# Optimization experiments

Hardware: AMD Instinct MI355X
Metric: run time of the kernel (lower is better)

## Reference

```python
import jax, jax.numpy as jnp
import numpy as np

B, S, D, H = 8, 1024, 1024, 16
DH = D // H  # 64

def setup_inputs() -> dict:
    key = jax.random.key(0)
    k1, k2, k3 = jax.random.split(key, 3)
    x = jax.random.normal(k1, (B, S, D), dtype=jnp.float32)
    mask = jnp.tril(jnp.ones((S, S), dtype=bool))[None, None]  # causal [1,1,S,S]
    W_qkv = jax.random.normal(k2, (D, 3 * D), dtype=jnp.float32) * 0.02
    W_out = jax.random.normal(k3, (D, D), dtype=jnp.float32) * 0.02
    return {"x": x, "mask": mask, "W_qkv": W_qkv, "W_out": W_out}

def reference(x, mask, W_qkv, W_out):
    qkv = jnp.einsum('bnd,de->bne', x, W_qkv)
    q, k, v = jnp.split(qkv, 3, axis=-1)
    # [b, h, n, dh]
    split_heads = lambda t: t.reshape(B, S, H, DH).transpose(0, 2, 1, 3)
    q, k, v = map(split_heads, (q, k, v))
    attn = jnp.einsum('bhnd,bhmd->bhnm', q, k) / jnp.sqrt(jnp.float32(DH))
    attn = jnp.where(mask, attn, 0.7 * jnp.finfo(attn.dtype).min)
    attn = jax.nn.softmax(attn.astype(jnp.float32), axis=-1).astype(x.dtype)
    out = jnp.einsum('bhnm,bhmd->bhnd', attn, v)
    out = out.transpose(0, 2, 1, 3).reshape(B, S, D)
    return jnp.einsum('bnd,de->bne', out, W_out)
```

## Files before the change

### kernel.cpp

```cpp
#include <hip/hip_runtime.h>
#include <stdint.h>

typedef __attribute__((ext_vector_type(8))) short short8;
typedef __attribute__((ext_vector_type(4))) float floatx4;

__device__ __forceinline__ unsigned short f2bf(float f) {
  union { float f; uint32_t u; } v; v.f = f;
  uint32_t u = v.u;
  return (unsigned short)((u + 0x7FFFu + ((u >> 16) & 1u)) >> 16);
}

__device__ __forceinline__ uint32_t fbits(float f) {
  union { float f; uint32_t u; } v; v.f = f; return v.u;
}
__device__ __forceinline__ uint32_t pkbf(float hi, float lo) {
  return __builtin_amdgcn_perm(fbits(hi), fbits(lo), 0x07060302u);
}

__device__ __forceinline__ void gl_lds16(const void* g, void* l) {
  __builtin_amdgcn_global_load_lds((__attribute__((address_space(1))) void*)g,
                                   (__attribute__((address_space(3))) void*)l,
                                   16, 0, 0);
}

__global__ __launch_bounds__(256) void prep_kernel(const float* __restrict__ x,
                                                   unsigned short* __restrict__ xb,
                                                   const float* __restrict__ Wqkv,
                                                   unsigned short* __restrict__ WqkvT,
                                                   const float* __restrict__ Wout,
                                                   unsigned short* __restrict__ WoutT) {
  __shared__ float tile[32][33];
  int id = blockIdx.x;
  if (id < 8192) {
    int i = id * 256 + threadIdx.x;
    float4 v = ((const float4*)x)[i];
    ushort4 o;
    o.x = f2bf(v.x); o.y = f2bf(v.y); o.z = f2bf(v.z); o.w = f2bf(v.w);
    ((ushort4*)xb)[i] = o;
    return;
  }
  id -= 8192;
  int bx = id & 127, r0 = (id >> 7) * 32;
  const int R = 1024;
  const float* in; unsigned short* out; int C;
  if (bx < 96) { in = Wqkv; out = WqkvT; C = 3072; }
  else         { in = Wout; out = WoutT; C = 1024; bx -= 96; }
  int c0 = bx * 32;
  int tx = threadIdx.x & 31;
  int ty = threadIdx.x >> 5;
  for (int i = ty; i < 32; i += 8)
    tile[i][tx] = in[(size_t)(r0 + i) * C + c0 + tx];
  __syncthreads();
  for (int i = ty; i < 32; i += 8)
    out[(size_t)(c0 + i) * R + r0 + tx] = f2bf(tile[tx][i]);
}

__global__ __launch_bounds__(256) void gemm_bt_kernel(const unsigned short* __restrict__ A,
                                                      const unsigned short* __restrict__ Bt,
                                                      int N, int mode,
                                                      unsigned short* __restrict__ qo,
                                                      unsigned short* __restrict__ ko,
                                                      unsigned short* __restrict__ vo,
                                                      float* __restrict__ fo) {
  const int Kd = 1024;
  __shared__ union {
    struct { unsigned short A[2][8192]; unsigned short B[2][8192]; } s;
    float cf[16384];
    unsigned short ch[32768];
  } sm;
  const int tid = threadIdx.x;
  const int w = tid >> 6, lane = tid & 63;
  const int quad = lane >> 4, l16 = lane & 15;
  const int l7 = l16 & 7;
  const int wm = w >> 1, wn = w & 1;
  const int m0 = blockIdx.y * 128, n0 = blockIdx.x * 128;
  const int tr = (mode == 0) && (n0 >= 2048);
  const int r8 = lane >> 3, ch = lane & 7;
  const int sw = (ch ^ r8) * 8;

  floatx4 acc[4][4];
#pragma unroll
  for (int i = 0; i < 4; ++i)
#pragma unroll
    for (int j = 0; j < 4; ++j)
      acc[i][j] = (floatx4){0.f, 0.f, 0.f, 0.f};

  auto stage = [&](int it, int buf) {
    const int k0 = it * 64;
#pragma unroll
    for (int i = 0; i < 4; ++i) {
      const int row = i * 32 + w * 8 + r8;
      gl_lds16(A + (size_t)(m0 + row) * Kd + k0 + sw, (char*)&sm.s.A[buf][0] + i * 4096 + w * 1024);
      gl_lds16(Bt + (size_t)(n0 + row) * Kd + k0 + sw, (char*)&sm.s.B[buf][0] + i * 4096 + w * 1024);
    }
  };

  stage(0, 0);
  __syncthreads();

  for (int it = 0; it < 16; ++it) {
    const int buf = it & 1;
    if (it < 15) stage(it + 1, buf ^ 1);
    const char* Ab = (const char*)&sm.s.A[buf][0];
    const char* Bb = (const char*)&sm.s.B[buf][0];
#pragma unroll
    for (int half = 0; half < 2; ++half) {
      short8 af[4], bf[4];
#pragma unroll
      for (int i = 0; i < 4; ++i)
        af[i] = *(const short8*)(Ab + (wm * 64 + i * 16 + l16) * 128 +
                                 (((half << 2) | quad) ^ l7) * 16);
#pragma unroll
      for (int j = 0; j < 4; ++j)
        bf[j] = *(const short8*)(Bb + (wn * 64 + j * 16 + l16) * 128 +
                                 (((half << 2) | quad) ^ l7) * 16);
      if (!tr) {
#pragma unroll
        for (int i = 0; i < 4; ++i)
#pragma unroll
          for (int j = 0; j < 4; ++j)
            acc[i][j] = __builtin_amdgcn_mfma_f32_16x16x32_bf16(af[i], bf[j], acc[i][j], 0, 0, 0);
      } else {
#pragma unroll
        for (int p = 0; p < 4; ++p)
#pragma unroll
          for (int q = 0; q < 4; ++q)
            acc[p][q] = __builtin_amdgcn_mfma_f32_16x16x32_bf16(bf[p], af[q], acc[p][q], 0, 0, 0);
      }
    }
    __syncthreads();
  }

  if (mode == 1) {
    float* Cs = sm.cf;
#pragma unroll
    for (int i = 0; i < 4; ++i)
#pragma unroll
      for (int j = 0; j < 4; ++j)
#pragma unroll
        for (int r = 0; r < 4; ++r) {
          int row = wm * 64 + i * 16 + quad * 4 + r;
          int col = wn * 64 + j * 16 + l16;
          Cs[row * 128 + (col ^ ((row & 7) << 2))] = acc[i][j][r];
        }
    __syncthreads();
#pragma unroll
    for (int c = 0; c < 16; ++c) {
      int idx = c * 256 + tid;
      int row = idx >> 5, fc = idx & 31;
      float4 v = *(const float4*)&sm.cf[row * 128 + ((fc ^ (row & 7)) << 2)];
      *(float4*)&fo[(size_t)(m0 + row) * N + n0 + fc * 4] = v;
    }
  } else {
    unsigned short* Cs = sm.ch;
    if (!tr) {
#pragma unroll
      for (int i = 0; i < 4; ++i)
#pragma unroll
        for (int j = 0; j < 4; ++j)
#pragma unroll
          for (int r = 0; r < 4; ++r) {
            int row = wm * 64 + i * 16 + quad * 4 + r;
            int col = wn * 64 + j * 16 + l16;
            Cs[row * 128 + (col ^ ((row & 7) << 3))] = f2bf(acc[i][j][r]);
          }
    } else {
#pragma unroll
      for (int p = 0; p < 4; ++p)
#pragma unroll
        for (int q = 0; q < 4; ++q)
#pragma unroll
          for (int r = 0; r < 4; ++r) {
            int row = wn * 64 + p * 16 + quad * 4 + r;
            int col = wm * 64 + q * 16 + l16;
            Cs[row * 128 + (col ^ ((row & 7) << 3))] = f2bf(acc[p][q][r]);
          }
    }
    __syncthreads();
    unsigned short* dst0 = (n0 < 1024) ? qo : ko;
#pragma unroll
    for (int c = 0; c < 8; ++c) {
      int idx = c * 256 + tid;
      int row = idx >> 4, lc = idx & 15;
      short8 v = *(const short8*)&sm.ch[row * 128 + ((lc ^ (row & 7)) << 3)];
      int col = lc * 8;
      if (!tr) {
        int m = m0 + row, n = n0 + col;
        int h = (n & 1023) >> 6, dh = n & 63;
        int bb = m >> 10, s = m & 1023;
        *(short8*)&dst0[(size_t)(bb * 16 + h) * 65536 + (size_t)s * 64 + dh] = v;
      } else {
        int n = n0 + row, m = m0 + col;
        int h = (n & 1023) >> 6, dh = n & 63;
        int bb = m >> 10, s0 = m & 1023;
        *(short8*)&vo[(size_t)(bb * 16 + h) * 65536 + (size_t)dh * 1024 + s0] = v;
      }
    }
  }
}

__global__ __launch_bounds__(256, 2) void attn_kernel(const unsigned short* __restrict__ Qb,
                                                      const unsigned short* __restrict__ Kb,
                                                      const unsigned short* __restrict__ VbT,
                                                      unsigned short* __restrict__ AOb) {
  __shared__ unsigned short Kt[2][4096];
  __shared__ unsigned short Vt[2][4096];
  const int tid = threadIdx.x;
  const int w = tid >> 6, lane = tid & 63;
  const int quad = lane >> 4, l16 = lane & 15;
  const int l7 = l16 & 7;
  const int id = blockIdx.x;
  const int by = id >> 2;
  const int p = id & 3;
  const int bb = by >> 4, hh = by & 15;
  const int qlo = p * 128 + w * 32;
  const int qhi = (7 - p) * 128 + w * 32;
  const unsigned short* Qp = Qb + (size_t)by * 65536;
  const unsigned short* Kp = Kb + (size_t)by * 65536;
  const unsigned short* Vp = VbT + (size_t)by * 65536;

  short8 bq[2][2][2];
#pragma unroll
  for (int g = 0; g < 2; ++g)
#pragma unroll
    for (int qt = 0; qt < 2; ++qt)
#pragma unroll
      for (int kh = 0; kh < 2; ++kh)
        bq[g][qt][kh] = *(const short8*)(Qp + (size_t)((g ? qhi : qlo) + qt * 16 + l16) * 64 +
                                         kh * 32 + quad * 8);

  floatx4 o[2][2][4];
  floatx4 ps[2][2];
#pragma unroll
  for (int g = 0; g < 2; ++g)
#pragma unroll
    for (int qt = 0; qt < 2; ++qt) {
      ps[g][qt] = (floatx4){0.f, 0.f, 0.f, 0.f};
#pragma unroll
      for (int dt = 0; dt < 4; ++dt) o[g][qt][dt] = (floatx4){0.f, 0.f, 0.f, 0.f};
    }

  short8 ones;
#pragma unroll
  for (int i = 0; i < 8; ++i) ones[i] = (short)0x3F80;

  const int T = 16 - 2 * p;
  const int r8 = lane >> 3, ch = lane & 7;
  const int sw8 = (ch ^ r8) * 8;

  auto stage = [&](int t, int buf) {
    const int n0 = t * 64;
#pragma unroll
    for (int i = 0; i < 2; ++i) {
      const int c = w * 2 + i;
      const int row = c * 8 + r8;
      gl_lds16(Kp + (size_t)(n0 + row) * 64 + sw8, (char*)&Kt[buf][0] + c * 1024);
      gl_lds16(Vp + (size_t)row * 1024 + n0 + sw8, (char*)&Vt[buf][0] + c * 1024);
    }
  };

  stage(0, 0);
  __syncthreads();

  for (int t = 0; t < T; ++t) {
    const int buf = t & 1;
    if (t + 1 < T) stage(t + 1, buf ^ 1);
    const int n0 = t * 64;
    const bool alo = (n0 <= qlo + 31), ahi = (n0 <= qhi + 31);
    if (alo | ahi) {
      const char* kbase = (const char*)&Kt[buf][0];
      const char* vbase = (const char*)&Vt[buf][0];
      short8 ak[4][2];
#pragma unroll
      for (int kt = 0; kt < 4; ++kt)
#pragma unroll
        for (int kh = 0; kh < 2; ++kh)
          ak[kt][kh] = *(const short8*)(kbase + (kt * 16 + l16) * 128 +
                                        (((kh << 2) | quad) ^ l7) * 16);
      union PaU { short8 v; uint32_t d[4]; };
      PaU pa[2][2][2];

      auto score = [&](int g, int qb) {
        const bool full = (n0 + 63 <= qb);
#pragma unroll
        for (int kt = 0; kt < 4; ++kt)
#pragma unroll
          for (int qt = 0; qt < 2; ++qt) {
            floatx4 s = (floatx4){0.f, 0.f, 0.f, 0.f};
            s = __builtin_amdgcn_mfma_f32_16x16x32_bf16(ak[kt][0], bq[g][qt][0], s, 0, 0, 0);
            s = __builtin_amdgcn_mfma_f32_16x16x32_bf16(ak[kt][1], bq[g][qt][1], s, 0, 0, 0);
            float f[4];
            if (full) {
#pragma unroll
              for (int r = 0; r < 4; ++r)
                f[r] = exp2f(fmaf(s[r], 0.18033688f, -11.5415603f));
            } else {
              const int query = qb + qt * 16 + l16;
#pragma unroll
              for (int r = 0; r < 4; ++r) {
                const int key = n0 + kt * 16 + quad * 4 + r;
                float e = exp2f(fmaf(s[r], 0.18033688f, -11.5415603f));
                f[r] = (key <= query) ? e : 0.0f;
              }
            }
            pa[g][qt][kt >> 1].d[(kt & 1) * 2 + 0] = pkbf(f[1], f[0]);
            pa[g][qt][kt >> 1].d[(kt & 1) * 2 + 1] = pkbf(f[3], f[2]);
          }
#pragma unroll
        for (int qt = 0; qt < 2; ++qt)
#pragma unroll
          for (int u = 0; u < 2; ++u)
            ps[g][qt] = __builtin_amdgcn_mfma_f32_16x16x32_bf16(pa[g][qt][u].v, ones, ps[g][qt], 0, 0, 0);
      };
      if (alo) score(0, qlo);
      if (ahi) score(1, qhi);

#pragma unroll
      for (int dt = 0; dt < 4; ++dt) {
        const int row128 = (dt * 16 + l16) * 128;
#pragma unroll
        for (int u = 0; u < 2; ++u) {
          union { short8 v8; ushort4 h[2]; } bv;
          bv.h[0] = *(const ushort4*)(vbase + row128 +
                                      (((u << 2) | (quad >> 1)) ^ l7) * 16 + (quad & 1) * 8);
          bv.h[1] = *(const ushort4*)(vbase + row128 +
                                      (((u << 2) | 2 | (quad >> 1)) ^ l7) * 16 + (quad & 1) * 8);
          if (alo) {
#pragma unroll
            for (int qt = 0; qt < 2; ++qt)
              o[0][qt][dt] = __builtin_amdgcn_mfma_f32_16x16x32_bf16(pa[0][qt][u].v, bv.v8, o[0][qt][dt], 0, 0, 0);
          }
          if (ahi) {
#pragma unroll
            for (int qt = 0; qt < 2; ++qt)
              o[1][qt][dt] = __builtin_amdgcn_mfma_f32_16x16x32_bf16(pa[1][qt][u].v, bv.v8, o[1][qt][dt], 0, 0, 0);
          }
        }
      }
    }
    __syncthreads();
  }

#pragma unroll
  for (int g = 0; g < 2; ++g) {
    const int qb = g ? qhi : qlo;
#pragma unroll
    for (int qt = 0; qt < 2; ++qt) {
      float inv[4];
#pragma unroll
      for (int r = 0; r < 4; ++r) inv[r] = 1.0f / ps[g][qt][r];
#pragma unroll
      for (int dt = 0; dt < 4; ++dt)
#pragma unroll
        for (int r = 0; r < 4; ++r) {
          int row = qb + qt * 16 + quad * 4 + r;
          AOb[(size_t)(bb * 1024 + row) * 1024 + hh * 64 + dt * 16 + l16] =
              f2bf(o[g][qt][dt][r] * inv[r]);
        }
    }
  }
}

extern "C" void kernel_launch(void* const* d_in, const int* in_sizes, int n_in,
                              void* d_out, int out_size, void* d_ws, size_t ws_size,
                              hipStream_t stream) {
  const float* x    = (const float*)d_in[0];
  const float* Wqkv = (const float*)d_in[2];
  const float* Wout = (const float*)d_in[3];
  float* out = (float*)d_out;

  unsigned short* xb    = (unsigned short*)d_ws;
  unsigned short* WqkvT = xb    + (size_t)8 * 1024 * 1024;
  unsigned short* WoutT = WqkvT + (size_t)3 * 1024 * 1024;
  unsigned short* Qb    = WoutT + (size_t)1024 * 1024;
  unsigned short* Kb    = Qb    + (size_t)8 * 1024 * 1024;
  unsigned short* VbT   = Kb    + (size_t)8 * 1024 * 1024;
  unsigned short* AOb   = VbT   + (size_t)8 * 1024 * 1024;

  prep_kernel<<<12288, 256, 0, stream>>>(x, xb, Wqkv, WqkvT, Wout, WoutT);
  gemm_bt_kernel<<<dim3(24, 64), 256, 0, stream>>>(xb, WqkvT, 3072, 0, Qb, Kb, VbT, nullptr);
  attn_kernel<<<512, 256, 0, stream>>>(Qb, Kb, VbT, AOb);
  gemm_bt_kernel<<<dim3(8, 64), 256, 0, stream>>>(AOb, WoutT, 1024, 1, nullptr, nullptr, nullptr, out);
}
```

Baseline: 231.7 us.

## Add dedicated 256x128-tile QKV GEMM kernel with 8 waves and phased MFMA schedule

Replaces the generic gemm_bt launch for the QKV projection with a specialized kernel that uses 512 threads and 256x128 output tiles. Each wave computes a 64x64 sub-tile, and the K loop is split into four phases. Global-to-LDS loads are interleaved between MFMA groups, with explicit barriers and setprio. The intent is more operand reuse per LDS load and better overlap of memory traffic with compute. The cost is higher register and LDS pressure, which may reduce occupancy, and fewer blocks in the grid.

```diff
diff --git a/kernel.cpp b/kernel.cpp
--- a/kernel.cpp
+++ b/kernel.cpp
@@ -199,6 +199,191 @@
   }
 }
 
+__global__ __launch_bounds__(512, 2) void gemm_qkv_kernel(const unsigned short* __restrict__ A,
+                                                          const unsigned short* __restrict__ Bt,
+                                                          unsigned short* __restrict__ qo,
+                                                          unsigned short* __restrict__ ko,
+                                                          unsigned short* __restrict__ vo) {
+  __shared__ union {
+    struct { unsigned short A[2][16384]; unsigned short B[2][8192]; } s;
+    unsigned short ch[49152];
+  } sm;
+  const int tid = threadIdx.x;
+  const int w = tid >> 6, lane = tid & 63;
+  const int quad = lane >> 4, l16 = lane & 15, l7 = l16 & 7;
+  const int wm = w >> 1, wn = w & 1;
+  const int m0 = blockIdx.y * 256, n0 = blockIdx.x * 128;
+  const bool tr = (n0 >= 2048);
+  const int r8 = lane >> 3, ch8 = lane & 7;
+  const int sw = (ch8 ^ r8) * 8;
+
+  floatx4 acc[16];
+#pragma unroll
+  for (int i = 0; i < 16; ++i) acc[i] = (floatx4){0.f, 0.f, 0.f, 0.f};
+
+  auto stageA = [&](int t, int buf) {
+    const int k0 = t * 64;
+#pragma unroll
+    for (int i = 0; i < 4; ++i) {
+      const int row = i * 64 + w * 8 + r8;
+      gl_lds16(A + (size_t)(m0 + row) * 1024 + k0 + sw,
+               (char*)&sm.s.A[buf][0] + (i * 64 + w * 8) * 128);
+    }
+  };
+  auto stageB = [&](int t, int buf) {
+    const int k0 = t * 64;
+#pragma unroll
+    for (int i = 0; i < 2; ++i) {
+      const int row = i * 64 + w * 8 + r8;
+      gl_lds16(Bt + (size_t)(n0 + row) * 1024 + k0 + sw,
+               (char*)&sm.s.B[buf][0] + (i * 64 + w * 8) * 128);
+    }
+  };
+
+  stageA(0, 0); stageB(0, 0);
+  stageA(1, 1); stageB(1, 1);
+  asm volatile("s_waitcnt vmcnt(6)" ::: "memory");
+  __builtin_amdgcn_s_barrier();
+
+  const int cK0 = (quad ^ l7) * 16;
+  const int cK1 = ((4 | quad) ^ l7) * 16;
+  const int arow = (wm * 64 + l16) * 128;
+  const int brow = (wn * 64 + l16) * 128;
+
+  short8 af[2][2];
+  short8 bf[2][2][2];
+
+#define MFMA8(MH, NH)                                                              \
+  do {                                                                             \
+    if (!tr) {                                                                     \
+      _Pragma("unroll") for (int kk = 0; kk < 2; ++kk)                             \
+      _Pragma("unroll") for (int m = 0; m < 2; ++m)                                \
+      _Pragma("unroll") for (int n = 0; n < 2; ++n)                                \
+        acc[((MH)*2 + m) * 4 + (NH)*2 + n] = __builtin_amdgcn_mfma_f32_16x16x32_bf16( \
+            af[m][kk], bf[NH][n][kk], acc[((MH)*2 + m) * 4 + (NH)*2 + n], 0, 0, 0);   \
+    } else {                                                                       \
+      _Pragma("unroll") for (int kk = 0; kk < 2; ++kk)                             \
+      _Pragma("unroll") for (int n = 0; n < 2; ++n)                                \
+      _Pragma("unroll") for (int m = 0; m < 2; ++m)                                \
+        acc[((NH)*2 + n) * 4 + (MH)*2 + m] = __builtin_amdgcn_mfma_f32_16x16x32_bf16( \
+            bf[NH][n][kk], af[m][kk], acc[((NH)*2 + n) * 4 + (MH)*2 + m], 0, 0, 0);   \
+    }                                                                              \
+  } while (0)
+
+  for (int t = 0; t < 16; ++t) {
+    const int buf = t & 1;
+    const char* Ab = (const char*)&sm.s.A[buf][0];
+    const char* Bb = (const char*)&sm.s.B[buf][0];
+
+#pragma unroll
+    for (int m = 0; m < 2; ++m) {
+      af[m][0] = *(const short8*)(Ab + arow + m * 2048 + cK0);
+      af[m][1] = *(const short8*)(Ab + arow + m * 2048 + cK1);
+    }
+#pragma unroll
+    for (int n = 0; n < 2; ++n) {
+      bf[0][n][0] = *(const short8*)(Bb + brow + n * 2048 + cK0);
+      bf[0][n][1] = *(const short8*)(Bb + brow + n * 2048 + cK1);
+    }
+    __builtin_amdgcn_s_barrier();
+    asm volatile("s_waitcnt lgkmcnt(0)" ::: "memory");
+    __builtin_amdgcn_s_setprio(1);
+    MFMA8(0, 0);
+    __builtin_amdgcn_s_setprio(0);
+    __builtin_amdgcn_sched_barrier(0);
+    __builtin_amdgcn_s_barrier();
+
+#pragma unroll
+    for (int n = 0; n < 2; ++n) {
+      bf[1][n][0] = *(const short8*)(Bb + brow + (2 + n) * 2048 + cK0);
+      bf[1][n][1] = *(const short8*)(Bb + brow + (2 + n) * 2048 + cK1);
+    }
+    __builtin_amdgcn_s_barrier();
+    asm volatile("s_waitcnt lgkmcnt(0)" ::: "memory");
+    __builtin_amdgcn_s_setprio(1);
+    MFMA8(0, 1);
+    __builtin_amdgcn_s_setprio(0);
+    __builtin_amdgcn_sched_barrier(0);
+    __builtin_amdgcn_s_barrier();
+
+#pragma unroll
+    for (int m = 0; m < 2; ++m) {
+      af[m][0] = *(const short8*)(Ab + arow + (2 + m) * 2048 + cK0);
+      af[m][1] = *(const short8*)(Ab + arow + (2 + m) * 2048 + cK1);
+    }
+    if (t < 14) stageB(t + 2, buf);
+    __builtin_amdgcn_s_barrier();
+    asm volatile("s_waitcnt lgkmcnt(0)" ::: "memory");
+    __builtin_amdgcn_s_setprio(1);
+    MFMA8(1, 1);
+    __builtin_amdgcn_s_setprio(0);
+    __builtin_amdgcn_sched_barrier(0);
+    __builtin_amdgcn_s_barrier();
+
+    if (t < 14) {
+      stageA(t + 2, buf);
+      asm volatile("s_waitcnt vmcnt(6)" ::: "memory");
+    } else {
+      asm volatile("s_waitcnt vmcnt(0)" ::: "memory");
+    }
+    __builtin_amdgcn_s_barrier();
+    __builtin_amdgcn_s_setprio(1);
+    MFMA8(1, 0);
+    __builtin_amdgcn_s_setprio(0);
+    __builtin_amdgcn_sched_barrier(0);
+    __builtin_amdgcn_s_barrier();
+  }
+#undef MFMA8
+
+  unsigned short* Cs = sm.ch;
+  if (!tr) {
+#pragma unroll
+    for (int mf = 0; mf < 4; ++mf)
+#pragma unroll
+      for (int nf = 0; nf < 4; ++nf)
+#pragma unroll
+        for (int r = 0; r < 4; ++r) {
+          int row = wm * 64 + mf * 16 + quad * 4 + r;
+          int col = wn * 64 + nf * 16 + l16;
+          Cs[row * 128 + (col ^ ((row & 7) << 3))] = f2bf(acc[mf * 4 + nf][r]);
+        }
+    __syncthreads();
+    unsigned short* dst0 = (n0 < 1024) ? qo : ko;
+#pragma unroll
+    for (int c = 0; c < 8; ++c) {
+      int idx = c * 512 + tid;
+      int row = idx >> 4, lc = idx & 15;
+      short8 v = *(const short8*)&Cs[row * 128 + ((lc ^ (row & 7)) << 3)];
+      int m = m0 + row, n = n0 + lc * 8;
+      int h = (n & 1023) >> 6, dh = n & 63;
+      int bb = m >> 10, s = m & 1023;
+      *(short8*)&dst0[(size_t)(bb * 16 + h) * 65536 + (size_t)s * 64 + dh] = v;
+    }
+  } else {
+#pragma unroll
+    for (int nf = 0; nf < 4; ++nf)
+#pragma unroll
+      for (int mf = 0; mf < 4; ++mf)
+#pragma unroll
+        for (int r = 0; r < 4; ++r) {
+          int row = wn * 64 + nf * 16 + quad * 4 + r;
+          int col = wm * 64 + mf * 16 + l16;
+          Cs[row * 256 + (col ^ ((row & 7) << 3))] = f2bf(acc[nf * 4 + mf][r]);
+        }
+    __syncthreads();
+#pragma unroll
+    for (int c = 0; c < 8; ++c) {
+      int idx = c * 512 + tid;
+      int row = idx >> 5, lc = idx & 31;
+      short8 v = *(const short8*)&Cs[row * 256 + ((lc ^ (row & 7)) << 3)];
+      int n = n0 + row, m = m0 + lc * 8;
+      int h = (n & 1023) >> 6, dh = n & 63;
+      int bb = m >> 10, s = m & 1023;
+      *(short8*)&vo[(size_t)(bb * 16 + h) * 65536 + (size_t)dh * 1024 + s] = v;
+    }
+  }
+}
+
 __global__ __launch_bounds__(256, 2) void attn_kernel(const unsigned short* __restrict__ Qb,
                                                       const unsigned short* __restrict__ Kb,
                                                       const unsigned short* __restrict__ VbT,
@@ -378,7 +563,7 @@
   unsigned short* AOb   = VbT   + (size_t)8 * 1024 * 1024;
 
   prep_kernel<<<12288, 256, 0, stream>>>(x, xb, Wqkv, WqkvT, Wout, WoutT);
-  gemm_bt_kernel<<<dim3(24, 64), 256, 0, stream>>>(xb, WqkvT, 3072, 0, Qb, Kb, VbT, nullptr);
+  gemm_qkv_kernel<<<dim3(24, 32), 512, 0, stream>>>(xb, WqkvT, Qb, Kb, VbT);
   attn_kernel<<<512, 256, 0, stream>>>(Qb, Kb, VbT, AOb);
   gemm_bt_kernel<<<dim3(8, 64), 256, 0, stream>>>(AOb, WoutT, 1024, 1, nullptr, nullptr, nullptr, out);
 }
```

Result: slower. 242.0 us (+4.4%).
